# Optimization experiments

Measured on AMD Instinct MI355X. Metric: run time of the kernel, lower is better.

The kernel has to match this reference:

```python
import jax, jax.numpy as jnp
import numpy as np

# Catmull-Rom basis: hermiteBasis @ tangent matrix (uniform spacing, deltas = 1,1,1)
_HERMITE = np.array([[2, -2, 1, 1], [-3, 3, -2, -1], [0, 0, 1, 0], [1, 0, 0, 0]], dtype=np.float32)
_CR = np.array([[0, 1, 0, 0], [0, 0, 1, 0], [-0.5, 0, 0.5, 0], [0, -0.5, 0, 0.5]], dtype=np.float32)
UNIFORM_BASIS = jnp.asarray(_HERMITE @ _CR)  # [[-0.5,1.5,-1.5,0.5],[1,-2.5,2,-0.5],[-0.5,0,0.5,0],[0,1,0,0]]

D, Z, Y, X, C = 16, 64, 128, 128, 2
N = 262144


def setup_inputs() -> dict:
    key = jax.random.key(0)
    k1, k2 = jax.random.split(key)
    u = jax.random.uniform(k1, (N, 3), dtype=jnp.float32)
    # zyx coords in [1, dim-3] so the 4-knot window stays mostly interior
    idx = u * jnp.array([Z - 4, Y - 4, X - 4], dtype=jnp.float32) + 1.0
    knots = jax.random.normal(k2, (D, Z, Y, X, C), dtype=jnp.float32)
    depth = jnp.float32(7.3)  # in (depths[0], depths[-1]) with depths = arange(1, D+1)
    return {"idx": idx, "knots": knots, "depth": depth}


def _spline_idx(coord, size):
    """coord: [N] float. Returns ([N,4] int knot indices, [N,4] spline weights)."""
    i0 = coord.astype(jnp.int32)                      # trunc == floor for positive coords
    s = jnp.clip(coord - i0.astype(coord.dtype), 0.0, 1.0)
    knot_idx = jnp.clip((i0 - 1)[:, None] + jnp.arange(4, dtype=jnp.int32)[None, :], 0, size - 1)
    # powers [s^3, s^2, s, 1] (explicit stack avoids 0**0 grad issues)
    powers = jnp.stack([s * s * s, s * s, s, jnp.ones_like(s)], axis=1)  # [N,4]
    return knot_idx, powers @ UNIFORM_BASIS


def reference(idx, knots, depth):
    D_, Z_, Y_, X_, _ = knots.shape
    n = idx.shape[0]
    depths = jnp.arange(1, D_ + 1, dtype=jnp.float32)  # uniform spacing -> time_diffs all 1
    ind = jnp.searchsorted(depths, depth, side='right')
    r = (depth - depths[ind - 1]) / (depths[ind] - depths[ind - 1])
    depth_coord = jnp.full((n,), (ind - 1).astype(jnp.float32) + r)

    idp, cd = _spline_idx(depth_coord, D_)
    iz, cz = _spline_idx(idx[:, 0], Z_)
    iy, cy = _spline_idx(idx[:, 1], Y_)
    ix, cx = _spline_idx(idx[:, 2], X_)

    # gather [N,4,4,4,4,C] knot neighborhood, then separable weighted reduction
    sel = knots[idp[:, :, None, None, None],
                iz[:, None, :, None, None],
                iy[:, None, None, :, None],
                ix[:, None, None, None, :]]
    return jnp.einsum('ndzyxc,nd,nz,ny,nx->nc', sel, cd, cz, cy, cx)
```

## Files before the change

### kernel.cpp

```cpp
#include <hip/hip_runtime.h>

#define Dd 16
#define Zd 64
#define Yd 128
#define Xd 128
#define Cd 2

__device__ __forceinline__ void spline_w(float coord, int size, int* idx4, float* w) {
    int i0 = (int)coord;
    float s = coord - (float)i0;
    s = fminf(fmaxf(s, 0.0f), 1.0f);
#pragma unroll
    for (int j = 0; j < 4; ++j) {
        int k = i0 - 1 + j;
        idx4[j] = min(max(k, 0), size - 1);
    }
    float s2 = s * s, s3 = s2 * s;
    w[0] = -0.5f * s3 + s2 - 0.5f * s;
    w[1] =  1.5f * s3 - 2.5f * s2 + 1.0f;
    w[2] = -1.5f * s3 + 2.0f * s2 + 0.5f * s;
    w[3] =  0.5f * s3 - 0.5f * s2;
}

__device__ __forceinline__ unsigned pack_bf16x2(float a, float b) {
    unsigned ua = __float_as_uint(a);
    unsigned ub = __float_as_uint(b);
    ua += 0x7fffu + ((ua >> 16) & 1u);
    ub += 0x7fffu + ((ub >> 16) & 1u);
    return (ua >> 16) | (ub & 0xffff0000u);
}

__global__ void depth_contract_bf16_kernel(const float* __restrict__ knots,
                                           const float* __restrict__ depth_p,
                                           uint4* __restrict__ Wv) {
    const int nv8 = Zd * Yd * Xd * Cd / 8;
    int t = blockIdx.x * blockDim.x + threadIdx.x;
    if (t >= nv8) return;

    int id[4]; float wd[4];
    spline_w(depth_p[0] - 1.0f, Dd, id, wd);

    const float4* kv = (const float4*)knots;
    const size_t slice4 = (size_t)Zd * Yd * Xd * Cd / 4;
    const size_t base = (size_t)t * 2;

    float4 r0 = make_float4(0.f, 0.f, 0.f, 0.f);
    float4 r1 = make_float4(0.f, 0.f, 0.f, 0.f);
#pragma unroll
    for (int j = 0; j < 4; ++j) {
        const float4* sp = kv + (size_t)id[j] * slice4 + base;
        float4 a = sp[0];
        float4 b = sp[1];
        float wj = wd[j];
        r0.x = fmaf(wj, a.x, r0.x); r0.y = fmaf(wj, a.y, r0.y);
        r0.z = fmaf(wj, a.z, r0.z); r0.w = fmaf(wj, a.w, r0.w);
        r1.x = fmaf(wj, b.x, r1.x); r1.y = fmaf(wj, b.y, r1.y);
        r1.z = fmaf(wj, b.z, r1.z); r1.w = fmaf(wj, b.w, r1.w);
    }
    uint4 o;
    o.x = pack_bf16x2(r0.x, r0.y);
    o.y = pack_bf16x2(r0.z, r0.w);
    o.z = pack_bf16x2(r1.x, r1.y);
    o.w = pack_bf16x2(r1.z, r1.w);
    Wv[t] = o;
}

__global__ void gather_eval_bf16_kernel(const float* __restrict__ idx,
                                        const unsigned* __restrict__ W,
                                        float* __restrict__ out, int n_pts) {
    int t = blockIdx.x * blockDim.x + threadIdx.x;
    int n = t >> 2;
    int q = t & 3;
    if (n >= n_pts) return;

    float zc = idx[n * 3 + 0];
    float yc = idx[n * 3 + 1];
    float xc = idx[n * 3 + 2];

    int iz[4], iy[4], ix[4];
    float wz[4], wy[4], wx[4];
    spline_w(zc, Zd, iz, wz);
    spline_w(yc, Yd, iy, wy);
    spline_w(xc, Xd, ix, wx);

    const int ixq = ix[q];
    const float wxq = wx[q];

    float r0 = 0.0f, r1 = 0.0f;
#pragma unroll
    for (int a = 0; a < 4; ++a) {
        const int zoff = iz[a] * (Yd * Xd);
#pragma unroll
        for (int b = 0; b < 4; ++b) {
            unsigned w = W[zoff + iy[b] * Xd + ixq];
            float c0 = __uint_as_float(w << 16);
            float c1 = __uint_as_float(w & 0xffff0000u);
            float wzy = wz[a] * wy[b];
            r0 = fmaf(wzy, c0, r0);
            r1 = fmaf(wzy, c1, r1);
        }
    }
    r0 *= wxq;
    r1 *= wxq;

    r0 += __shfl_xor(r0, 1); r0 += __shfl_xor(r0, 2);
    r1 += __shfl_xor(r1, 1); r1 += __shfl_xor(r1, 2);

    if (q == 0) {
        float2 o; o.x = r0; o.y = r1;
        ((float2*)out)[n] = o;
    }
}

__global__ void fused_kernel(const float* __restrict__ idx,
                             const float* __restrict__ knots,
                             const float* __restrict__ depth_p,
                             float* __restrict__ out, int n_pts) {
    int n = blockIdx.x * blockDim.x + threadIdx.x;
    if (n >= n_pts) return;
    int id[4]; float wd[4];
    spline_w(depth_p[0] - 1.0f, Dd, id, wd);
    int iz[4], iy[4], ix[4];
    float wz[4], wy[4], wx[4];
    spline_w(idx[n * 3 + 0], Zd, iz, wz);
    spline_w(idx[n * 3 + 1], Yd, iy, wy);
    spline_w(idx[n * 3 + 2], Xd, ix, wx);
    float acc0 = 0.0f, acc1 = 0.0f;
    for (int dd = 0; dd < 4; ++dd) {
        const float* base = knots + (size_t)id[dd] * Zd * Yd * Xd * Cd;
        float d0 = 0.0f, d1 = 0.0f;
        for (int a = 0; a < 4; ++a)
            for (int bb = 0; bb < 4; ++bb) {
                const float2* row = (const float2*)(base + ((size_t)(iz[a] * Yd + iy[bb]) * Xd) * Cd);
                float r0 = 0.0f, r1 = 0.0f;
                for (int qq = 0; qq < 4; ++qq) {
                    float2 v = row[ix[qq]];
                    r0 = fmaf(wx[qq], v.x, r0);
                    r1 = fmaf(wx[qq], v.y, r1);
                }
                float wzy = wz[a] * wy[bb];
                d0 = fmaf(wzy, r0, d0);
                d1 = fmaf(wzy, r1, d1);
            }
        acc0 = fmaf(wd[dd], d0, acc0);
        acc1 = fmaf(wd[dd], d1, acc1);
    }
    out[n * 2 + 0] = acc0;
    out[n * 2 + 1] = acc1;
}

extern "C" void kernel_launch(void* const* d_in, const int* in_sizes, int n_in,
                              void* d_out, int out_size, void* d_ws, size_t ws_size,
                              hipStream_t stream) {
    const float* idx   = (const float*)d_in[0];
    const float* knots = (const float*)d_in[1];
    const float* depth = (const float*)d_in[2];
    float* out = (float*)d_out;
    const int n_pts = in_sizes[0] / 3;

    const size_t wBytes = (size_t)Zd * Yd * Xd * Cd * 2;
    if (ws_size >= wBytes) {
        unsigned* W = (unsigned*)d_ws;
        const int nv8 = Zd * Yd * Xd * Cd / 8;
        depth_contract_bf16_kernel<<<(nv8 + 255) / 256, 256, 0, stream>>>(knots, depth, (uint4*)W);
        const int nthreads = n_pts * 4;
        gather_eval_bf16_kernel<<<(nthreads + 255) / 256, 256, 0, stream>>>(idx, W, out, n_pts);
    } else {
        fused_kernel<<<(n_pts + 255) / 256, 256, 0, stream>>>(idx, knots, depth, out, n_pts);
    }
}
```

Baseline: 194.9 us.

## Store depth-contracted grid in 2x4x2 brick layout for gather locality

The depth-contracted bf16 intermediate grid is now written in a bricked (Morton-like) order: 2 z by 4 y by 2 x cells per 64-byte brick. The gather kernel computes brick addresses so that the 4x4 z/y neighborhood of each point touches fewer cache lines. The contraction kernel now reads scattered float2 values instead of contiguous float4 vectors. A launch-bounds hint is also added to the gather kernel.

```diff
diff --git a/kernel.cpp b/kernel.cpp
--- a/kernel.cpp
+++ b/kernel.cpp
@@ -5,6 +5,7 @@
 #define Yd 128
 #define Xd 128
 #define Cd 2
+
 
 __device__ __forceinline__ void spline_w(float coord, int size, int* idx4, float* w) {
     int i0 = (int)coord;
@@ -30,44 +31,44 @@
     return (ua >> 16) | (ub & 0xffff0000u);
 }
 
-__global__ void depth_contract_bf16_kernel(const float* __restrict__ knots,
-                                           const float* __restrict__ depth_p,
-                                           uint4* __restrict__ Wv) {
-    const int nv8 = Zd * Yd * Xd * Cd / 8;
+__global__ void depth_contract_brick_kernel(const float* __restrict__ knots,
+                                            const float* __restrict__ depth_p,
+                                            uint4* __restrict__ Wv) {
+    const int nv4 = Zd * Yd * Xd / 4;
     int t = blockIdx.x * blockDim.x + threadIdx.x;
-    if (t >= nv8) return;
+    if (t >= nv4) return;
 
     int id[4]; float wd[4];
     spline_w(depth_p[0] - 1.0f, Dd, id, wd);
 
-    const float4* kv = (const float4*)knots;
-    const size_t slice4 = (size_t)Zd * Yd * Xd * Cd / 4;
-    const size_t base = (size_t)t * 2;
+    const float2* __restrict__ k2 = (const float2*)knots;
+    const int slice = Zd * Yd * Xd;
 
-    float4 r0 = make_float4(0.f, 0.f, 0.f, 0.f);
-    float4 r1 = make_float4(0.f, 0.f, 0.f, 0.f);
+    unsigned packed[4];
 #pragma unroll
-    for (int j = 0; j < 4; ++j) {
-        const float4* sp = kv + (size_t)id[j] * slice4 + base;
-        float4 a = sp[0];
-        float4 b = sp[1];
-        float wj = wd[j];
-        r0.x = fmaf(wj, a.x, r0.x); r0.y = fmaf(wj, a.y, r0.y);
-        r0.z = fmaf(wj, a.z, r0.z); r0.w = fmaf(wj, a.w, r0.w);
-        r1.x = fmaf(wj, b.x, r1.x); r1.y = fmaf(wj, b.y, r1.y);
-        r1.z = fmaf(wj, b.z, r1.z); r1.w = fmaf(wj, b.w, r1.w);
+    for (int e = 0; e < 4; ++e) {
+        int u = t * 4 + e;
+        int z = ((u >> 15) << 1) | ((u >> 3) & 1);
+        int y = (((u >> 10) & 31) << 2) | ((u >> 1) & 3);
+        int x = (((u >> 4) & 63) << 1) | (u & 1);
+        int lin = (z * Yd + y) * Xd + x;
+        float r0 = 0.f, r1 = 0.f;
+#pragma unroll
+        for (int j = 0; j < 4; ++j) {
+            float2 v = k2[id[j] * slice + lin];
+            r0 = fmaf(wd[j], v.x, r0);
+            r1 = fmaf(wd[j], v.y, r1);
+        }
+        packed[e] = pack_bf16x2(r0, r1);
     }
-    uint4 o;
-    o.x = pack_bf16x2(r0.x, r0.y);
-    o.y = pack_bf16x2(r0.z, r0.w);
-    o.z = pack_bf16x2(r1.x, r1.y);
-    o.w = pack_bf16x2(r1.z, r1.w);
+    uint4 o; o.x = packed[0]; o.y = packed[1]; o.z = packed[2]; o.w = packed[3];
     Wv[t] = o;
 }
 
-__global__ void gather_eval_bf16_kernel(const float* __restrict__ idx,
-                                        const unsigned* __restrict__ W,
-                                        float* __restrict__ out, int n_pts) {
+__global__ __launch_bounds__(256, 8)
+void gather_eval_brick_kernel(const float* __restrict__ idx,
+                              const unsigned* __restrict__ W,
+                              float* __restrict__ out, int n_pts) {
     int t = blockIdx.x * blockDim.x + threadIdx.x;
     int n = t >> 2;
     int q = t & 3;
@@ -83,16 +84,22 @@
     spline_w(yc, Yd, iy, wy);
     spline_w(xc, Xd, ix, wx);
 
-    const int ixq = ix[q];
+    const int xq = ix[q];
+    const int xcomp = ((xq >> 1) << 4) | (xq & 1);
     const float wxq = wx[q];
+
+    int za[4], yb_[4];
+#pragma unroll
+    for (int a = 0; a < 4; ++a) za[a]  = ((iz[a] >> 1) << 15) | ((iz[a] & 1) << 3);
+#pragma unroll
+    for (int b = 0; b < 4; ++b) yb_[b] = ((iy[b] >> 2) << 10) | ((iy[b] & 3) << 1);
 
     float r0 = 0.0f, r1 = 0.0f;
 #pragma unroll
     for (int a = 0; a < 4; ++a) {
-        const int zoff = iz[a] * (Yd * Xd);
 #pragma unroll
         for (int b = 0; b < 4; ++b) {
-            unsigned w = W[zoff + iy[b] * Xd + ixq];
+            unsigned w = W[za[a] + yb_[b] + xcomp];
             float c0 = __uint_as_float(w << 16);
             float c1 = __uint_as_float(w & 0xffff0000u);
             float wzy = wz[a] * wy[b];
@@ -161,10 +168,10 @@
     const size_t wBytes = (size_t)Zd * Yd * Xd * Cd * 2;
     if (ws_size >= wBytes) {
         unsigned* W = (unsigned*)d_ws;
-        const int nv8 = Zd * Yd * Xd * Cd / 8;
-        depth_contract_bf16_kernel<<<(nv8 + 255) / 256, 256, 0, stream>>>(knots, depth, (uint4*)W);
+        const int nv4 = Zd * Yd * Xd / 4;
+        depth_contract_brick_kernel<<<(nv4 + 255) / 256, 256, 0, stream>>>(knots, depth, (uint4*)W);
         const int nthreads = n_pts * 4;
-        gather_eval_bf16_kernel<<<(nthreads + 255) / 256, 256, 0, stream>>>(idx, W, out, n_pts);
+        gather_eval_brick_kernel<<<(nthreads + 255) / 256, 256, 0, stream>>>(idx, W, out, n_pts);
     } else {
         fused_kernel<<<(n_pts + 255) / 256, 256, 0, stream>>>(idx, knots, depth, out, n_pts);
     }
```

Result: no change. 195.3 us (+0.2%).
